# Optimization experiments

Measured on AMD Instinct MI355X. Metric: run time of the kernel, lower is better.

Reference implementation:

```python
import jax, jax.numpy as jnp
import numpy as np
from jax import lax


def quick_gelu(x):
    return x * jax.nn.sigmoid(1.702 * x)


def setup_inputs() -> dict:
    key = jax.random.key(0)
    ks = jax.random.split(key, 12)
    B, H, W, C, D, M = 32, 56, 56, 192, 64, 8
    g = lambda k, shape, s: (jax.random.normal(k, shape, jnp.float32) * s)
    return {
        "x": jax.random.normal(ks[0], (B, H, W, C), jnp.float32),
        "W1": g(ks[1], (64, C), 0.05),
        "b1": jnp.zeros((64,), jnp.float32),
        "W2": g(ks[2], (64, 64), 0.05),
        "b2": jnp.zeros((64,), jnp.float32),
        "mask_token": g(ks[3], (M, 64), 0.05),
        "Wh": g(ks[4], (D * D * 9, 64), 0.02),
        "bh": g(ks[5], (D * D * 9,), 0.02),
        "Wd": g(ks[6], (D, C), 0.05),
        "bd": jnp.zeros((D,), jnp.float32),
        "Wu": g(ks[7], (C, D), 0.02),
        "bu": jnp.zeros((C,), jnp.float32),
    }


def reference(x, W1, b1, W2, b2, mask_token, Wh, bh, Wd, bd, Wu, bu):
    B, H, W_, C = x.shape
    D = Wd.shape[0]
    M = mask_token.shape[0]
    # meta_net: Linear -> ReLU -> Linear, [B,H,W,64]
    pf = jax.nn.relu(jnp.einsum("bhwc,kc->bhwk", x, W1) + b1)
    pf = jnp.einsum("bhwk,jk->bhwj", pf, W2) + b2
    # mask routing: [M,B,H,W], softmax over spatial positions
    mask = jnp.einsum("bhwk,mk->mbhw", pf, mask_token)
    mask = jax.nn.softmax(mask.reshape(M, B, -1), axis=-1).reshape(M, B, H, W_)
    # sum_m mask[m][...,None]*pf, then sum over H,W -> [B,64]
    mwf = (mask.sum(0)[..., None] * pf).sum(axis=(1, 2))
    # hypernet: per-sample conv weights [B,D,D,3,3]
    conv_w = (jnp.einsum("bk,ok->bo", mwf, Wh) + bh).reshape(B, D, D, 3, 3)
    # adapter_down + QuickGELU, [B,D,H,W]
    xd = jnp.einsum("bhwc,dc->bhwd", x, Wd) + bd
    xp = quick_gelu(xd.transpose(0, 3, 1, 2))

    def conv1(xi, wi):  # xi [D,H,W], wi [D,D,3,3]
        return lax.conv_general_dilated(xi[None], wi, (1, 1), [(1, 1), (1, 1)])[0]

    xc = jax.vmap(conv1)(xp, conv_w)  # [B,D,H,W]
    xd2 = quick_gelu(xc.transpose(0, 2, 3, 1))  # [B,H,W,D]
    # dropout(p=0.1) is identity in eval mode
    xu = jnp.einsum("bhwd,cd->bhwc", xd2, Wu) + bu
    return xu + x
```

## Files before the change

kernel.cpp:

```cpp
#include <hip/hip_runtime.h>

typedef unsigned short ushort_t;
typedef short bf16x8 __attribute__((ext_vector_type(8)));
typedef float f32x4 __attribute__((ext_vector_type(4)));

#define MFMA(a, b, c) __builtin_amdgcn_mfma_f32_16x16x32_bf16(a, b, c, 0, 0, 0)

#define B_    32
#define HW_   3136
#define NPOS  100352

__device__ __forceinline__ float bf2f(unsigned short h) {
    return __uint_as_float(((unsigned int)h) << 16);
}
__device__ __forceinline__ unsigned short f2bf(float f) {
    unsigned int u = __float_as_uint(f);
    u += 0x7FFFu + ((u >> 16) & 1u);
    return (unsigned short)(u >> 16);
}
__device__ __forceinline__ float qgelu(float v) {
    return v / (1.0f + __expf(-1.702f * v));
}
__device__ __forceinline__ void unpack8(uint4 v, float* f) {
    f[0] = bf2f((unsigned short)(v.x & 0xffff)); f[1] = bf2f((unsigned short)(v.x >> 16));
    f[2] = bf2f((unsigned short)(v.y & 0xffff)); f[3] = bf2f((unsigned short)(v.y >> 16));
    f[4] = bf2f((unsigned short)(v.z & 0xffff)); f[5] = bf2f((unsigned short)(v.z >> 16));
    f[6] = bf2f((unsigned short)(v.w & 0xffff)); f[7] = bf2f((unsigned short)(v.w >> 16));
}

__global__ __launch_bounds__(256) void k0_prep(
    const float* __restrict__ W1, const float* __restrict__ W2,
    const float* __restrict__ mtok, const float* __restrict__ Wd,
    const float* __restrict__ Wu,
    ushort_t* __restrict__ w1f, ushort_t* __restrict__ wdf,
    ushort_t* __restrict__ w2f, ushort_t* __restrict__ mtf,
    ushort_t* __restrict__ wuf)
{
    const int gid = blockIdx.x * 256 + threadIdx.x;
    const int stride = gridDim.x * 256;
    for (int i = gid; i < 12288; i += stride) {
        int j = i & 7, lane = (i >> 3) & 63, nt = (i >> 9) & 3, kc = i >> 11;
        int n = nt * 16 + (lane & 15), k = kc * 32 + (lane >> 4) * 8 + j;
        w1f[i] = f2bf(W1[n * 192 + k]);
        wdf[i] = f2bf(Wd[n * 192 + k]);
    }
    for (int i = gid; i < 4096; i += stride) {
        int j = i & 7, lane = (i >> 3) & 63, nt = (i >> 9) & 3, kc = i >> 11;
        int n = nt * 16 + (lane & 15), k = kc * 32 + (lane >> 4) * 8 + j;
        w2f[i] = f2bf(W2[n * 64 + k]);
    }
    for (int i = gid; i < 1024; i += stride) {
        int j = i & 7, lane = (i >> 3) & 63, kc = i >> 9;
        int n = lane & 15, k = kc * 32 + (lane >> 4) * 8 + j;
        mtf[i] = (n < 8) ? f2bf(mtok[n * 64 + k]) : (ushort_t)0;
    }
    for (int i = gid; i < 12288; i += stride) {
        int j = i & 7, lane = (i >> 3) & 63, g = i >> 9;
        int nt = g % 12, kc = g / 12;
        int n = nt * 16 + (lane & 15), k = kc * 32 + (lane >> 4) * 8 + j;
        wuf[i] = f2bf(Wu[n * 64 + k]);
    }
}

__global__ __launch_bounds__(64, 2) void k1_meta_adapter(
    const float* __restrict__ x, const float* __restrict__ b1,
    const float* __restrict__ b2, const float* __restrict__ bd,
    const ushort_t* __restrict__ w1f, const ushort_t* __restrict__ wdf,
    const ushort_t* __restrict__ w2f, const ushort_t* __restrict__ mtf,
    ushort_t* __restrict__ pf2g, ushort_t* __restrict__ xpg,
    float* __restrict__ Lg)
{
    __shared__ ushort_t buf[16 * 72];

    const int lane = threadIdx.x;
    const int col = lane & 15, q = lane >> 4;
    const int posBase = blockIdx.x * 64;

    float bias1[4], biasd[4], bias2[4];
    #pragma unroll
    for (int nt = 0; nt < 4; nt++) {
        bias1[nt] = b1[nt * 16 + col];
        biasd[nt] = bd[nt * 16 + col];
        bias2[nt] = b2[nt * 16 + col];
    }

    f32x4 acc1[4][4], acc3[4][4];
    #pragma unroll
    for (int m = 0; m < 4; m++)
        #pragma unroll
        for (int nt = 0; nt < 4; nt++) { acc1[m][nt] = (f32x4)0.0f; acc3[m][nt] = (f32x4)0.0f; }

    #pragma unroll
    for (int kc = 0; kc < 6; kc++) {
        bf16x8 A[4];
        #pragma unroll
        for (int m = 0; m < 4; m++) {
            const float4* gp = (const float4*)(x +
                (size_t)(posBase + m * 16 + col) * 192 + kc * 32 + q * 8);
            float4 v0 = gp[0], v1 = gp[1];
            A[m][0] = (short)f2bf(v0.x); A[m][1] = (short)f2bf(v0.y);
            A[m][2] = (short)f2bf(v0.z); A[m][3] = (short)f2bf(v0.w);
            A[m][4] = (short)f2bf(v1.x); A[m][5] = (short)f2bf(v1.y);
            A[m][6] = (short)f2bf(v1.z); A[m][7] = (short)f2bf(v1.w);
        }
        #pragma unroll
        for (int nt = 0; nt < 4; nt++) {
            bf16x8 B1 = *(const bf16x8*)(w1f + ((kc * 4 + nt) * 64 + lane) * 8);
            #pragma unroll
            for (int m = 0; m < 4; m++) acc1[m][nt] = MFMA(A[m], B1, acc1[m][nt]);
            bf16x8 Bd = *(const bf16x8*)(wdf + ((kc * 4 + nt) * 64 + lane) * 8);
            #pragma unroll
            for (int m = 0; m < 4; m++) acc3[m][nt] = MFMA(A[m], Bd, acc3[m][nt]);
        }
    }

    #pragma unroll
    for (int m = 0; m < 4; m++) {
        const int rowBase = posBase + m * 16;

        #pragma unroll
        for (int nt = 0; nt < 4; nt++)
            #pragma unroll
            for (int r = 0; r < 4; r++) {
                float v = acc1[m][nt][r] + bias1[nt];
                v = v > 0.0f ? v : 0.0f;
                buf[(q * 4 + r) * 72 + nt * 16 + col] = f2bf(v);
            }

        f32x4 acc2[4];
        #pragma unroll
        for (int nt = 0; nt < 4; nt++) acc2[nt] = (f32x4)0.0f;
        #pragma unroll
        for (int kc = 0; kc < 2; kc++) {
            bf16x8 A2 = *(const bf16x8*)&buf[col * 72 + kc * 32 + q * 8];
            #pragma unroll
            for (int nt = 0; nt < 4; nt++) {
                bf16x8 B2 = *(const bf16x8*)(w2f + ((kc * 4 + nt) * 64 + lane) * 8);
                acc2[nt] = MFMA(A2, B2, acc2[nt]);
            }
        }

        #pragma unroll
        for (int nt = 0; nt < 4; nt++)
            #pragma unroll
            for (int r = 0; r < 4; r++) {
                float v = qgelu(acc3[m][nt][r] + biasd[nt]);
                buf[(q * 4 + r) * 72 + nt * 16 + col] = f2bf(v);
            }

        #pragma unroll
        for (int t = 0; t < 2; t++) {
            int idx = lane + t * 64;
            int pos = idx >> 3, c8 = idx & 7;
            uint4 vx = *(const uint4*)&buf[pos * 72 + c8 * 8];
            *(uint4*)(xpg + ((size_t)(rowBase + pos)) * 64 + c8 * 8) = vx;
        }

        #pragma unroll
        for (int nt = 0; nt < 4; nt++)
            #pragma unroll
            for (int r = 0; r < 4; r++)
                buf[(q * 4 + r) * 72 + nt * 16 + col] = f2bf(acc2[nt][r] + bias2[nt]);

        f32x4 Lacc = (f32x4)0.0f;
        #pragma unroll
        for (int kc = 0; kc < 2; kc++) {
            bf16x8 A3 = *(const bf16x8*)&buf[col * 72 + kc * 32 + q * 8];
            bf16x8 Bm = *(const bf16x8*)(mtf + (kc * 64 + lane) * 8);
            Lacc = MFMA(A3, Bm, Lacc);
        }
        if (col < 8) {
            #pragma unroll
            for (int r = 0; r < 4; r++)
                Lg[((size_t)(rowBase + q * 4 + r)) * 8 + col] = Lacc[r];
        }

        #pragma unroll
        for (int t = 0; t < 2; t++) {
            int idx = lane + t * 64;
            int pos = idx >> 3, c8 = idx & 7;
            uint4 vp = *(const uint4*)&buf[pos * 72 + c8 * 8];
            *(uint4*)(pf2g + ((size_t)(rowBase + pos)) * 64 + c8 * 8) = vp;
        }
    }
}

__global__ __launch_bounds__(256) void k2a_partial(
    const float* __restrict__ Lg, float* __restrict__ Pmax, float* __restrict__ Psum)
{
    __shared__ float wred[4][8];
    __shared__ float Msh[8];

    const int tid = threadIdx.x;
    const int b = blockIdx.x >> 3, sl = blockIdx.x & 7;
    const int lane = tid & 63, wv = tid >> 6;
    const float* Lb = Lg + ((size_t)b * HW_ + (size_t)sl * 392) * 8;

    float l0[8], l1[8];
    {
        const float4* p = (const float4*)(Lb + (size_t)tid * 8);
        float4 a = p[0], c = p[1];
        l0[0] = a.x; l0[1] = a.y; l0[2] = a.z; l0[3] = a.w;
        l0[4] = c.x; l0[5] = c.y; l0[6] = c.z; l0[7] = c.w;
    }
    if (tid < 136) {
        const float4* p = (const float4*)(Lb + (size_t)(tid + 256) * 8);
        float4 a = p[0], c = p[1];
        l1[0] = a.x; l1[1] = a.y; l1[2] = a.z; l1[3] = a.w;
        l1[4] = c.x; l1[5] = c.y; l1[6] = c.z; l1[7] = c.w;
    } else {
        #pragma unroll
        for (int m = 0; m < 8; m++) l1[m] = -1e30f;
    }

    float lm[8];
    #pragma unroll
    for (int m = 0; m < 8; m++) {
        float v = fmaxf(l0[m], l1[m]);
        for (int off = 32; off > 0; off >>= 1) v = fmaxf(v, __shfl_down(v, off));
        lm[m] = v;
    }
    if (lane == 0) {
        #pragma unroll
        for (int m = 0; m < 8; m++) wred[wv][m] = lm[m];
    }
    __syncthreads();
    if (tid < 8)
        Msh[tid] = fmaxf(fmaxf(wred[0][tid], wred[1][tid]), fmaxf(wred[2][tid], wred[3][tid]));
    __syncthreads();

    float s[8];
    #pragma unroll
    for (int m = 0; m < 8; m++)
        s[m] = __expf(l0[m] - Msh[m]) + __expf(l1[m] - Msh[m]);
    #pragma unroll
    for (int m = 0; m < 8; m++) {
        float v = s[m];
        for (int off = 32; off > 0; off >>= 1) v += __shfl_down(v, off);
        s[m] = v;
    }
    __syncthreads();
    if (lane == 0) {
        #pragma unroll
        for (int m = 0; m < 8; m++) wred[wv][m] = s[m];
    }
    __syncthreads();
    if (tid < 8) {
        Psum[((size_t)b * 8 + sl) * 8 + tid] =
            wred[0][tid] + wred[1][tid] + wred[2][tid] + wred[3][tid];
        Pmax[((size_t)b * 8 + sl) * 8 + tid] = Msh[tid];
    }
}

__global__ __launch_bounds__(256) void k2b_combine(
    const float* __restrict__ Pmax, const float* __restrict__ Psum,
    float* __restrict__ smxg, float* __restrict__ sinvg, float* __restrict__ mwfg)
{
    const int tid = threadIdx.x;
    const int b = tid >> 3, m = tid & 7;
    float M = -1e30f;
    #pragma unroll
    for (int sl = 0; sl < 8; sl++)
        M = fmaxf(M, Pmax[((size_t)b * 8 + sl) * 8 + m]);
    float S = 0.0f;
    #pragma unroll
    for (int sl = 0; sl < 8; sl++)
        S += Psum[((size_t)b * 8 + sl) * 8 + m] * __expf(Pmax[((size_t)b * 8 + sl) * 8 + m] - M);
    smxg[tid] = M;
    sinvg[tid] = 1.0f / S;
    for (int i = tid; i < 2048; i += 256) mwfg[i] = 0.0f;
}

__global__ __launch_bounds__(256) void k2c_mwf(
    const float* __restrict__ Lg, const ushort_t* __restrict__ pf2g,
    const float* __restrict__ smxg, const float* __restrict__ sinvg,
    float* __restrict__ mwfg)
{
    __shared__ float ms[392];
    __shared__ float sred[32 * 64];

    const int tid = threadIdx.x;
    const int b = blockIdx.x >> 3, sl = blockIdx.x & 7;
    const size_t base = (size_t)b * HW_ + (size_t)sl * 392;

    float smx[8], sinv[8];
    #pragma unroll
    for (int m = 0; m < 8; m++) {
        smx[m] = smxg[b * 8 + m];
        sinv[m] = sinvg[b * 8 + m];
    }

    for (int lp = tid; lp < 392; lp += 256) {
        const float4* p = (const float4*)(Lg + (base + lp) * 8);
        float4 a = p[0], c = p[1];
        ms[lp] = __expf(a.x - smx[0]) * sinv[0] + __expf(a.y - smx[1]) * sinv[1]
               + __expf(a.z - smx[2]) * sinv[2] + __expf(a.w - smx[3]) * sinv[3]
               + __expf(c.x - smx[4]) * sinv[4] + __expf(c.y - smx[5]) * sinv[5]
               + __expf(c.z - smx[6]) * sinv[6] + __expf(c.w - smx[7]) * sinv[7];
    }
    __syncthreads();

    const int part = tid >> 3, kg = tid & 7;
    float a8[8];
    #pragma unroll
    for (int j = 0; j < 8; j++) a8[j] = 0.0f;
    for (int lp = part; lp < 392; lp += 32) {
        float w = ms[lp];
        uint4 v = *(const uint4*)(pf2g + (base + lp) * 64 + kg * 8);
        float f[8]; unpack8(v, f);
        #pragma unroll
        for (int j = 0; j < 8; j++) a8[j] += w * f[j];
    }
    #pragma unroll
    for (int j = 0; j < 8; j++) sred[part * 64 + kg * 8 + j] = a8[j];
    __syncthreads();
    if (tid < 64) {
        float s = 0.0f;
        #pragma unroll
        for (int pt = 0; pt < 32; pt++) s += sred[pt * 64 + tid];
        atomicAdd(&mwfg[b * 64 + tid], s);
    }
}

__global__ __launch_bounds__(256) void k3_hypernet(
    const float* __restrict__ mwfg, const float* __restrict__ Whg,
    const float* __restrict__ bhg, ushort_t* __restrict__ cwb)
{
    __shared__ float mwfs[32 * 64];
    const int tid = threadIdx.x;
    for (int i = tid; i < 2048; i += 256) mwfs[i] = mwfg[i];
    __syncthreads();

    const int op = blockIdx.x * 64 + (tid >> 2);
    const int bq = tid & 3;
    const int j = op & 7, lane = (op >> 3) & 63, nt = (op >> 9) & 3;
    const int kc = (op >> 11) & 1, tap = op >> 12;
    const int oc = nt * 16 + (lane & 15);
    const int ic = kc * 32 + (lane >> 4) * 8 + j;
    const int o = oc * 576 + ic * 9 + tap;

    float wreg[64];
    const float4* src = (const float4*)(Whg + (size_t)o * 64);
    #pragma unroll
    for (int t = 0; t < 16; t++) {
        float4 v = src[t];
        wreg[t * 4 + 0] = v.x; wreg[t * 4 + 1] = v.y;
        wreg[t * 4 + 2] = v.z; wreg[t * 4 + 3] = v.w;
    }
    const float bias = bhg[o];
    #pragma unroll
    for (int i = 0; i < 8; i += 2) {
        int b0 = bq * 8 + i, b1 = b0 + 1;
        float a0 = bias, a1 = bias;
        #pragma unroll
        for (int k = 0; k < 64; k++) {
            a0 += mwfs[b0 * 64 + k] * wreg[k];
            a1 += mwfs[b1 * 64 + k] * wreg[k];
        }
        cwb[(size_t)b0 * 36864 + op] = f2bf(a0);
        cwb[(size_t)b1 * 36864 + op] = f2bf(a1);
    }
}

__global__ __launch_bounds__(256, 4) void k4_conv(
    const ushort_t* __restrict__ xpg, const ushort_t* __restrict__ cwb,
    ushort_t* __restrict__ xd2g)
{
    __shared__ ushort_t xs[2 * 232 * 40];

    const int tid = threadIdx.x;
    const int bid = blockIdx.x;
    const int swz = (bid & 7) * 112 + (bid >> 3);
    const int b = swz / 28, yt = swz % 28, y0 = yt * 2;

    for (int u = tid; u < 1856; u += 256) {
        int r = u / 464, rem = u % 464, c = rem >> 3, c8 = rem & 7;
        int gy = y0 - 1 + r, gx = c - 1;
        uint4 v = make_uint4(0, 0, 0, 0);
        if (gy >= 0 && gy < 56 && gx >= 0 && gx < 56)
            v = *(const uint4*)(xpg + ((size_t)b * HW_ + gy * 56 + gx) * 64 + c8 * 8);
        int kc = c8 >> 2, q = c8 & 3;
        *(uint4*)&xs[kc * 9280 + (r * 58 + c) * 40 + q * 8] = v;
    }
    __syncthreads();

    const int lane = tid & 63, wv = tid >> 6;
    const int col = lane & 15, q = lane >> 4;

    int abase[7];
    #pragma unroll
    for (int t = 0; t < 7; t++) {
        int p = t * 16 + col;
        int row = p / 56, cc = p - row * 56;
        abase[t] = ((row * 58 + cc) * 40 + q * 8) * 2;
    }

    f32x4 acc[7];
    #pragma unroll
    for (int t = 0; t < 7; t++) acc[t] = (f32x4)0.0f;

    const ushort_t* wbase = cwb + (size_t)b * 36864;
    #pragma unroll
    for (int tap = 0; tap < 9; tap++) {
        const int dy = tap / 3, dx = tap % 3;
        const int toff = (dy * 58 + dx) * 80;
        bf16x8 Bf0 = *(const bf16x8*)(wbase + tap * 4096 + ((0 * 4 + wv) * 64 + lane) * 8);
        bf16x8 Bf1 = *(const bf16x8*)(wbase + tap * 4096 + ((1 * 4 + wv) * 64 + lane) * 8);
        #pragma unroll
        for (int t = 0; t < 7; t++) {
            bf16x8 A0 = *(const bf16x8*)((const char*)xs + abase[t] + toff);
            bf16x8 A1 = *(const bf16x8*)((const char*)xs + 18560 + abase[t] + toff);
            acc[t] = MFMA(A0, Bf0, acc[t]);
            acc[t] = MFMA(A1, Bf1, acc[t]);
        }
    }
    __syncthreads();

    #pragma unroll
    for (int t = 0; t < 7; t++)
        #pragma unroll
        for (int r = 0; r < 4; r++)
            xs[(t * 16 + q * 4 + r) * 72 + wv * 16 + col] = f2bf(qgelu(acc[t][r]));
    __syncthreads();

    for (int u = tid; u < 896; u += 256) {
        int pos = u >> 3, c8 = u & 7;
        uint4 v = *(const uint4*)&xs[pos * 72 + c8 * 8];
        size_t gpos = (size_t)b * HW_ + (size_t)y0 * 56 + pos;
        *(uint4*)(xd2g + gpos * 64 + c8 * 8) = v;
    }
}

__global__ __launch_bounds__(256, 4) void k5_up_res(
    const ushort_t* __restrict__ xd2g, const ushort_t* __restrict__ wuf,
    const float* __restrict__ bu, const float* __restrict__ xg,
    float* __restrict__ outg)
{
    __shared__ ushort_t xds[64 * 72];
    __shared__ ushort_t wsh[12288];

    const int tid = threadIdx.x;
    const size_t posBase = (size_t)blockIdx.x * 64;

    {
        uint4* d = (uint4*)wsh;
        const uint4* s = (const uint4*)wuf;
        for (int u = tid; u < 1536; u += 256) d[u] = s[u];
    }
    #pragma unroll
    for (int t = 0; t < 2; t++) {
        int u = tid + t * 256;
        int pos = u >> 3, c8 = u & 7;
        uint4 v = *(const uint4*)(xd2g + (posBase + pos) * 64 + c8 * 8);
        *(uint4*)&xds[pos * 72 + c8 * 8] = v;
    }
    __syncthreads();

    const int lane = tid & 63, wv = tid >> 6;
    const int col = lane & 15, q = lane >> 4;

    bf16x8 A[2];
    #pragma unroll
    for (int kc = 0; kc < 2; kc++)
        A[kc] = *(const bf16x8*)&xds[(wv * 16 + col) * 72 + kc * 32 + q * 8];

    f32x4 acc[12];
    #pragma unroll
    for (int nt = 0; nt < 12; nt++) acc[nt] = (f32x4)0.0f;
    #pragma unroll
    for (int kc = 0; kc < 2; kc++)
        #pragma unroll
        for (int nt = 0; nt < 12; nt++) {
            bf16x8 B = *(const bf16x8*)&wsh[((kc * 12 + nt) * 64 + lane) * 8];
            acc[nt] = MFMA(A[kc], B, acc[nt]);
        }

    #pragma unroll
    for (int nt = 0; nt < 12; nt++) {
        float bias = bu[nt * 16 + col];
        #pragma unroll
        for (int r = 0; r < 4; r++) {
            size_t off = (posBase + wv * 16 + q * 4 + r) * 192 + nt * 16 + col;
            outg[off] = acc[nt][r] + bias + xg[off];
        }
    }
}

extern "C" void kernel_launch(void* const* d_in, const int* in_sizes, int n_in,
                              void* d_out, int out_size, void* d_ws, size_t ws_size,
                              hipStream_t stream) {
    const float* x    = (const float*)d_in[0];
    const float* W1   = (const float*)d_in[1];
    const float* b1   = (const float*)d_in[2];
    const float* W2   = (const float*)d_in[3];
    const float* b2   = (const float*)d_in[4];
    const float* mtok = (const float*)d_in[5];
    const float* Wh   = (const float*)d_in[6];
    const float* bh   = (const float*)d_in[7];
    const float* Wd   = (const float*)d_in[8];
    const float* bd   = (const float*)d_in[9];
    const float* Wu   = (const float*)d_in[10];
    const float* bu   = (const float*)d_in[11];
    float* out = (float*)d_out;

    char* ws = (char*)d_ws;
    ushort_t* pf2 = (ushort_t*)ws;
    ushort_t* xp  = (ushort_t*)(ws + 12845056);
    ushort_t* xd2 = pf2;
    ushort_t* cwb = (ushort_t*)(ws + 25690112);
    float*    mwf = (float*)(ws + 28049408);
    float*    Lg  = (float*)(ws + 28057600);
    ushort_t* w1f = (ushort_t*)(ws + 31268864);
    ushort_t* wdf = (ushort_t*)(ws + 31293440);
    ushort_t* w2f = (ushort_t*)(ws + 31318016);
    ushort_t* mtf = (ushort_t*)(ws + 31326208);
    ushort_t* wuf = (ushort_t*)(ws + 31328256);
    float*    Pmax= (float*)(ws + 31352832);
    float*    Psum= (float*)(ws + 31361024);
    float*    smxg= (float*)(ws + 31369216);
    float*    sinvg=(float*)(ws + 31370240);

    k0_prep<<<48, 256, 0, stream>>>(W1, W2, mtok, Wd, Wu, w1f, wdf, w2f, mtf, wuf);
    k1_meta_adapter<<<1568, 64, 0, stream>>>(x, b1, b2, bd, w1f, wdf, w2f, mtf,
                                             pf2, xp, Lg);
    k2a_partial<<<256, 256, 0, stream>>>(Lg, Pmax, Psum);
    k2b_combine<<<1, 256, 0, stream>>>(Pmax, Psum, smxg, sinvg, mwf);
    k2c_mwf<<<256, 256, 0, stream>>>(Lg, pf2, smxg, sinvg, mwf);
    k3_hypernet<<<576, 256, 0, stream>>>(mwf, Wh, bh, cwb);
    k4_conv<<<896, 256, 0, stream>>>(xp, cwb, xd2);
    k5_up_res<<<1568, 256, 0, stream>>>(xd2, wuf, bu, x, out);
}
```

Baseline: 241.3 us.

## Split meta/adapter and up-projection across four waves; fold softmax combine kernel

k1 moves from one 64-thread wave per 64 positions to four waves, each owning a 16-column output slice, with weights held in registers and intermediates passed through shared memory. The tiny k2b combine kernel is removed: k2c now recomputes the per-batch max and sum from the partials, and the mwf zeroing moves into k2a. k5 drops its shared-memory staging and has each wave load weights and activations straight from global memory, with the register tile reshaped to 4 row blocks by 3 column blocks. In exchange, every wave in k1 re-reads the same x rows (four times the L2 traffic for x, with repeated bf16 conversion), and k5 loses its shared weight staging.

```diff
diff --git a/kernel.cpp b/kernel.cpp
--- a/kernel.cpp
+++ b/kernel.cpp
@@ -62,7 +62,7 @@
     }
 }
 
-__global__ __launch_bounds__(64, 2) void k1_meta_adapter(
+__global__ __launch_bounds__(256, 2) void k1_meta_adapter(
     const float* __restrict__ x, const float* __restrict__ b1,
     const float* __restrict__ b2, const float* __restrict__ bd,
     const ushort_t* __restrict__ w1f, const ushort_t* __restrict__ wdf,
@@ -70,25 +70,34 @@
     ushort_t* __restrict__ pf2g, ushort_t* __restrict__ xpg,
     float* __restrict__ Lg)
 {
-    __shared__ ushort_t buf[16 * 72];
-
-    const int lane = threadIdx.x;
+    __shared__ ushort_t pf1s[64 * 72];
+    __shared__ ushort_t pf2s[64 * 72];
+    __shared__ ushort_t xps[64 * 72];
+
+    const int tid = threadIdx.x;
+    const int lane = tid & 63, wv = tid >> 6;
     const int col = lane & 15, q = lane >> 4;
     const int posBase = blockIdx.x * 64;
 
-    float bias1[4], biasd[4], bias2[4];
-    #pragma unroll
-    for (int nt = 0; nt < 4; nt++) {
-        bias1[nt] = b1[nt * 16 + col];
-        biasd[nt] = bd[nt * 16 + col];
-        bias2[nt] = b2[nt * 16 + col];
-    }
-
-    f32x4 acc1[4][4], acc3[4][4];
-    #pragma unroll
-    for (int m = 0; m < 4; m++)
-        #pragma unroll
-        for (int nt = 0; nt < 4; nt++) { acc1[m][nt] = (f32x4)0.0f; acc3[m][nt] = (f32x4)0.0f; }
+    bf16x8 B1r[6], Bdr[6], B2r[2], Bmr[2];
+    #pragma unroll
+    for (int kc = 0; kc < 6; kc++) {
+        B1r[kc] = *(const bf16x8*)(w1f + ((kc * 4 + wv) * 64 + lane) * 8);
+        Bdr[kc] = *(const bf16x8*)(wdf + ((kc * 4 + wv) * 64 + lane) * 8);
+    }
+    #pragma unroll
+    for (int kc = 0; kc < 2; kc++) {
+        B2r[kc] = *(const bf16x8*)(w2f + ((kc * 4 + wv) * 64 + lane) * 8);
+        Bmr[kc] = *(const bf16x8*)(mtf + (kc * 64 + lane) * 8);
+    }
+
+    const float bias1 = b1[wv * 16 + col];
+    const float biasd = bd[wv * 16 + col];
+    const float bias2 = b2[wv * 16 + col];
+
+    f32x4 acc1[4], acc3[4];
+    #pragma unroll
+    for (int m = 0; m < 4; m++) { acc1[m] = (f32x4)0.0f; acc3[m] = (f32x4)0.0f; }
 
     #pragma unroll
     for (int kc = 0; kc < 6; kc++) {
@@ -104,89 +113,69 @@
             A[m][6] = (short)f2bf(v1.z); A[m][7] = (short)f2bf(v1.w);
         }
         #pragma unroll
-        for (int nt = 0; nt < 4; nt++) {
-            bf16x8 B1 = *(const bf16x8*)(w1f + ((kc * 4 + nt) * 64 + lane) * 8);
-            #pragma unroll
-            for (int m = 0; m < 4; m++) acc1[m][nt] = MFMA(A[m], B1, acc1[m][nt]);
-            bf16x8 Bd = *(const bf16x8*)(wdf + ((kc * 4 + nt) * 64 + lane) * 8);
-            #pragma unroll
-            for (int m = 0; m < 4; m++) acc3[m][nt] = MFMA(A[m], Bd, acc3[m][nt]);
+        for (int m = 0; m < 4; m++) {
+            acc1[m] = MFMA(A[m], B1r[kc], acc1[m]);
+            acc3[m] = MFMA(A[m], Bdr[kc], acc3[m]);
         }
     }
 
     #pragma unroll
-    for (int m = 0; m < 4; m++) {
-        const int rowBase = posBase + m * 16;
-
-        #pragma unroll
-        for (int nt = 0; nt < 4; nt++)
-            #pragma unroll
-            for (int r = 0; r < 4; r++) {
-                float v = acc1[m][nt][r] + bias1[nt];
-                v = v > 0.0f ? v : 0.0f;
-                buf[(q * 4 + r) * 72 + nt * 16 + col] = f2bf(v);
-            }
-
-        f32x4 acc2[4];
-        #pragma unroll
-        for (int nt = 0; nt < 4; nt++) acc2[nt] = (f32x4)0.0f;
-        #pragma unroll
-        for (int kc = 0; kc < 2; kc++) {
-            bf16x8 A2 = *(const bf16x8*)&buf[col * 72 + kc * 32 + q * 8];
-            #pragma unroll
-            for (int nt = 0; nt < 4; nt++) {
-                bf16x8 B2 = *(const bf16x8*)(w2f + ((kc * 4 + nt) * 64 + lane) * 8);
-                acc2[nt] = MFMA(A2, B2, acc2[nt]);
-            }
+    for (int m = 0; m < 4; m++)
+        #pragma unroll
+        for (int r = 0; r < 4; r++)
+            pf1s[(m * 16 + q * 4 + r) * 72 + wv * 16 + col] =
+                f2bf(fmaxf(acc1[m][r] + bias1, 0.0f));
+    __syncthreads();
+
+    f32x4 acc2[4];
+    #pragma unroll
+    for (int m = 0; m < 4; m++) acc2[m] = (f32x4)0.0f;
+    #pragma unroll
+    for (int kc = 0; kc < 2; kc++) {
+        #pragma unroll
+        for (int m = 0; m < 4; m++) {
+            bf16x8 A2 = *(const bf16x8*)&pf1s[(m * 16 + col) * 72 + kc * 32 + q * 8];
+            acc2[m] = MFMA(A2, B2r[kc], acc2[m]);
         }
-
-        #pragma unroll
-        for (int nt = 0; nt < 4; nt++)
-            #pragma unroll
-            for (int r = 0; r < 4; r++) {
-                float v = qgelu(acc3[m][nt][r] + biasd[nt]);
-                buf[(q * 4 + r) * 72 + nt * 16 + col] = f2bf(v);
-            }
-
-        #pragma unroll
-        for (int t = 0; t < 2; t++) {
-            int idx = lane + t * 64;
-            int pos = idx >> 3, c8 = idx & 7;
-            uint4 vx = *(const uint4*)&buf[pos * 72 + c8 * 8];
-            *(uint4*)(xpg + ((size_t)(rowBase + pos)) * 64 + c8 * 8) = vx;
+    }
+
+    #pragma unroll
+    for (int m = 0; m < 4; m++)
+        #pragma unroll
+        for (int r = 0; r < 4; r++) {
+            xps[(m * 16 + q * 4 + r) * 72 + wv * 16 + col] =
+                f2bf(qgelu(acc3[m][r] + biasd));
+            pf2s[(m * 16 + q * 4 + r) * 72 + wv * 16 + col] =
+                f2bf(acc2[m][r] + bias2);
         }
-
-        #pragma unroll
-        for (int nt = 0; nt < 4; nt++)
-            #pragma unroll
-            for (int r = 0; r < 4; r++)
-                buf[(q * 4 + r) * 72 + nt * 16 + col] = f2bf(acc2[nt][r] + bias2[nt]);
-
-        f32x4 Lacc = (f32x4)0.0f;
-        #pragma unroll
-        for (int kc = 0; kc < 2; kc++) {
-            bf16x8 A3 = *(const bf16x8*)&buf[col * 72 + kc * 32 + q * 8];
-            bf16x8 Bm = *(const bf16x8*)(mtf + (kc * 64 + lane) * 8);
-            Lacc = MFMA(A3, Bm, Lacc);
-        }
-        if (col < 8) {
-            #pragma unroll
-            for (int r = 0; r < 4; r++)
-                Lg[((size_t)(rowBase + q * 4 + r)) * 8 + col] = Lacc[r];
-        }
-
-        #pragma unroll
-        for (int t = 0; t < 2; t++) {
-            int idx = lane + t * 64;
-            int pos = idx >> 3, c8 = idx & 7;
-            uint4 vp = *(const uint4*)&buf[pos * 72 + c8 * 8];
-            *(uint4*)(pf2g + ((size_t)(rowBase + pos)) * 64 + c8 * 8) = vp;
-        }
+    __syncthreads();
+
+    f32x4 Lacc = (f32x4)0.0f;
+    #pragma unroll
+    for (int kc = 0; kc < 2; kc++) {
+        bf16x8 A3 = *(const bf16x8*)&pf2s[(wv * 16 + col) * 72 + kc * 32 + q * 8];
+        Lacc = MFMA(A3, Bmr[kc], Lacc);
+    }
+    if (col < 8) {
+        #pragma unroll
+        for (int r = 0; r < 4; r++)
+            Lg[((size_t)(posBase + wv * 16 + q * 4 + r)) * 8 + col] = Lacc[r];
+    }
+
+    #pragma unroll
+    for (int t = 0; t < 2; t++) {
+        int u = tid + t * 256;
+        int pos = u >> 3, c8 = u & 7;
+        uint4 vx = *(const uint4*)&xps[pos * 72 + c8 * 8];
+        *(uint4*)(xpg + ((size_t)(posBase + pos)) * 64 + c8 * 8) = vx;
+        uint4 vp = *(const uint4*)&pf2s[pos * 72 + c8 * 8];
+        *(uint4*)(pf2g + ((size_t)(posBase + pos)) * 64 + c8 * 8) = vp;
     }
 }
 
 __global__ __launch_bounds__(256) void k2a_partial(
-    const float* __restrict__ Lg, float* __restrict__ Pmax, float* __restrict__ Psum)
+    const float* __restrict__ Lg, float* __restrict__ Pmax, float* __restrict__ Psum,
+    float* __restrict__ mwfg)
 {
     __shared__ float wred[4][8];
     __shared__ float Msh[8];
@@ -195,6 +184,9 @@
     const int b = blockIdx.x >> 3, sl = blockIdx.x & 7;
     const int lane = tid & 63, wv = tid >> 6;
     const float* Lb = Lg + ((size_t)b * HW_ + (size_t)sl * 392) * 8;
+
+    if (blockIdx.x == 0)
+        for (int i = tid; i < 2048; i += 256) mwfg[i] = 0.0f;
 
     float l0[8], l1[8];
     {
@@ -252,28 +244,9 @@
     }
 }
 
-__global__ __launch_bounds__(256) void k2b_combine(
-    const float* __restrict__ Pmax, const float* __restrict__ Psum,
-    float* __restrict__ smxg, float* __restrict__ sinvg, float* __restrict__ mwfg)
-{
-    const int tid = threadIdx.x;
-    const int b = tid >> 3, m = tid & 7;
-    float M = -1e30f;
-    #pragma unroll
-    for (int sl = 0; sl < 8; sl++)
-        M = fmaxf(M, Pmax[((size_t)b * 8 + sl) * 8 + m]);
-    float S = 0.0f;
-    #pragma unroll
-    for (int sl = 0; sl < 8; sl++)
-        S += Psum[((size_t)b * 8 + sl) * 8 + m] * __expf(Pmax[((size_t)b * 8 + sl) * 8 + m] - M);
-    smxg[tid] = M;
-    sinvg[tid] = 1.0f / S;
-    for (int i = tid; i < 2048; i += 256) mwfg[i] = 0.0f;
-}
-
 __global__ __launch_bounds__(256) void k2c_mwf(
     const float* __restrict__ Lg, const ushort_t* __restrict__ pf2g,
-    const float* __restrict__ smxg, const float* __restrict__ sinvg,
+    const float* __restrict__ Pmax, const float* __restrict__ Psum,
     float* __restrict__ mwfg)
 {
     __shared__ float ms[392];
@@ -286,8 +259,16 @@
     float smx[8], sinv[8];
     #pragma unroll
     for (int m = 0; m < 8; m++) {
-        smx[m] = smxg[b * 8 + m];
-        sinv[m] = sinvg[b * 8 + m];
+        float M = -1e30f;
+        #pragma unroll
+        for (int s2 = 0; s2 < 8; s2++)
+            M = fmaxf(M, Pmax[((size_t)b * 8 + s2) * 8 + m]);
+        float S = 0.0f;
+        #pragma unroll
+        for (int s2 = 0; s2 < 8; s2++)
+            S += Psum[((size_t)b * 8 + s2) * 8 + m] *
+                 __expf(Pmax[((size_t)b * 8 + s2) * 8 + m] - M);
+        smx[m] = M; sinv[m] = 1.0f / S;
     }
 
     for (int lp = tid; lp < 392; lp += 256) {
@@ -431,59 +412,58 @@
     }
 }
 
-__global__ __launch_bounds__(256, 4) void k5_up_res(
+__global__ __launch_bounds__(256, 2) void k5_up_res(
     const ushort_t* __restrict__ xd2g, const ushort_t* __restrict__ wuf,
     const float* __restrict__ bu, const float* __restrict__ xg,
     float* __restrict__ outg)
 {
-    __shared__ ushort_t xds[64 * 72];
-    __shared__ ushort_t wsh[12288];
-
     const int tid = threadIdx.x;
-    const size_t posBase = (size_t)blockIdx.x * 64;
-
-    {
-        uint4* d = (uint4*)wsh;
-        const uint4* s = (const uint4*)wuf;
-        for (int u = tid; u < 1536; u += 256) d[u] = s[u];
-    }
-    #pragma unroll
-    for (int t = 0; t < 2; t++) {
-        int u = tid + t * 256;
-        int pos = u >> 3, c8 = u & 7;
-        uint4 v = *(const uint4*)(xd2g + (posBase + pos) * 64 + c8 * 8);
-        *(uint4*)&xds[pos * 72 + c8 * 8] = v;
-    }
-    __syncthreads();
-
     const int lane = tid & 63, wv = tid >> 6;
     const int col = lane & 15, q = lane >> 4;
-
-    bf16x8 A[2];
+    const size_t posBase = (size_t)blockIdx.x * 64;
+
+    bf16x8 Bw[2][3];
     #pragma unroll
     for (int kc = 0; kc < 2; kc++)
-        A[kc] = *(const bf16x8*)&xds[(wv * 16 + col) * 72 + kc * 32 + q * 8];
-
-    f32x4 acc[12];
-    #pragma unroll
-    for (int nt = 0; nt < 12; nt++) acc[nt] = (f32x4)0.0f;
+        #pragma unroll
+        for (int nt = 0; nt < 3; nt++)
+            Bw[kc][nt] = *(const bf16x8*)(wuf + ((kc * 12 + wv * 3 + nt) * 64 + lane) * 8);
+
+    bf16x8 A[4][2];
+    #pragma unroll
+    for (int m = 0; m < 4; m++)
+        #pragma unroll
+        for (int kc = 0; kc < 2; kc++)
+            A[m][kc] = *(const bf16x8*)(xd2g +
+                (posBase + m * 16 + col) * 64 + kc * 32 + q * 8);
+
+    float biasu[3];
+    #pragma unroll
+    for (int nt = 0; nt < 3; nt++) biasu[nt] = bu[(wv * 3 + nt) * 16 + col];
+
+    f32x4 acc[4][3];
+    #pragma unroll
+    for (int m = 0; m < 4; m++)
+        #pragma unroll
+        for (int nt = 0; nt < 3; nt++) acc[m][nt] = (f32x4)0.0f;
+
     #pragma unroll
     for (int kc = 0; kc < 2; kc++)
         #pragma unroll
-        for (int nt = 0; nt < 12; nt++) {
-            bf16x8 B = *(const bf16x8*)&wsh[((kc * 12 + nt) * 64 + lane) * 8];
-            acc[nt] = MFMA(A[kc], B, acc[nt]);
-        }
-
-    #pragma unroll
-    for (int nt = 0; nt < 12; nt++) {
-        float bias = bu[nt * 16 + col];
-        #pragma unroll
-        for (int r = 0; r < 4; r++) {
-            size_t off = (posBase + wv * 16 + q * 4 + r) * 192 + nt * 16 + col;
-            outg[off] = acc[nt][r] + bias + xg[off];
-        }
-    }
+        for (int m = 0; m < 4; m++)
+            #pragma unroll
+            for (int nt = 0; nt < 3; nt++)
+                acc[m][nt] = MFMA(A[m][kc], Bw[kc][nt], acc[m][nt]);
+
+    #pragma unroll
+    for (int m = 0; m < 4; m++)
+        #pragma unroll
+        for (int nt = 0; nt < 3; nt++)
+            #pragma unroll
+            for (int r = 0; r < 4; r++) {
+                size_t off = (posBase + m * 16 + q * 4 + r) * 192 + (wv * 3 + nt) * 16 + col;
+                outg[off] = acc[m][nt][r] + biasu[nt] + xg[off];
+            }
 }
 
 extern "C" void kernel_launch(void* const* d_in, const int* in_sizes, int n_in,
@@ -517,15 +497,12 @@
     ushort_t* wuf = (ushort_t*)(ws + 31328256);
     float*    Pmax= (float*)(ws + 31352832);
     float*    Psum= (float*)(ws + 31361024);
-    float*    smxg= (float*)(ws + 31369216);
-    float*    sinvg=(float*)(ws + 31370240);
 
     k0_prep<<<48, 256, 0, stream>>>(W1, W2, mtok, Wd, Wu, w1f, wdf, w2f, mtf, wuf);
-    k1_meta_adapter<<<1568, 64, 0, stream>>>(x, b1, b2, bd, w1f, wdf, w2f, mtf,
-                                             pf2, xp, Lg);
-    k2a_partial<<<256, 256, 0, stream>>>(Lg, Pmax, Psum);
-    k2b_combine<<<1, 256, 0, stream>>>(Pmax, Psum, smxg, sinvg, mwf);
-    k2c_mwf<<<256, 256, 0, stream>>>(Lg, pf2, smxg, sinvg, mwf);
+    k1_meta_adapter<<<1568, 256, 0, stream>>>(x, b1, b2, bd, w1f, wdf, w2f, mtf,
+                                              pf2, xp, Lg);
+    k2a_partial<<<256, 256, 0, stream>>>(Lg, Pmax, Psum, mwf);
+    k2c_mwf<<<256, 256, 0, stream>>>(Lg, pf2, Pmax, Psum, mwf);
     k3_hypernet<<<576, 256, 0, stream>>>(mwf, Wh, bh, cwb);
     k4_conv<<<896, 256, 0, stream>>>(xp, cwb, xd2);
     k5_up_res<<<1568, 256, 0, stream>>>(xd2, wuf, bu, x, out);
```

New measurement: 256.4 us. 1.06x slower.

## Fuse block-local softmax and weighted pf reduction into meta kernel

Applied to the files above, without the earlier changes.

The meta/adapter kernel now keeps its 64 positions' pf2 tile and routing logits in shared memory. It computes a block-local online-softmax max and sum, plus a per-mask weighted pf sum via MFMA, and writes only small per-block partials. A single combine kernel rescales those partials into mwf. This drops the global pf2 and logit round trips and replaces three launches with one. The cost is more LDS per block and the removal of the occupancy hint, and the exp weights are rounded to bf16 before the MFMA.

```diff
diff --git a/kernel.cpp b/kernel.cpp
--- a/kernel.cpp
+++ b/kernel.cpp
@@ -20,12 +20,6 @@
 }
 __device__ __forceinline__ float qgelu(float v) {
     return v / (1.0f + __expf(-1.702f * v));
-}
-__device__ __forceinline__ void unpack8(uint4 v, float* f) {
-    f[0] = bf2f((unsigned short)(v.x & 0xffff)); f[1] = bf2f((unsigned short)(v.x >> 16));
-    f[2] = bf2f((unsigned short)(v.y & 0xffff)); f[3] = bf2f((unsigned short)(v.y >> 16));
-    f[4] = bf2f((unsigned short)(v.z & 0xffff)); f[5] = bf2f((unsigned short)(v.z >> 16));
-    f[6] = bf2f((unsigned short)(v.w & 0xffff)); f[7] = bf2f((unsigned short)(v.w >> 16));
 }
 
 __global__ __launch_bounds__(256) void k0_prep(
@@ -62,19 +56,23 @@
     }
 }
 
-__global__ __launch_bounds__(64, 2) void k1_meta_adapter(
+__global__ __launch_bounds__(64) void k1_meta_adapter(
     const float* __restrict__ x, const float* __restrict__ b1,
     const float* __restrict__ b2, const float* __restrict__ bd,
     const ushort_t* __restrict__ w1f, const ushort_t* __restrict__ wdf,
     const ushort_t* __restrict__ w2f, const ushort_t* __restrict__ mtf,
-    ushort_t* __restrict__ pf2g, ushort_t* __restrict__ xpg,
-    float* __restrict__ Lg)
+    ushort_t* __restrict__ xpg, float* __restrict__ Tg, float* __restrict__ MSg)
 {
     __shared__ ushort_t buf[16 * 72];
+    __shared__ ushort_t pf2t[64 * 72];
+    __shared__ ushort_t wsh[16 * 72];
+    __shared__ float    Lsh[64 * 8];
 
     const int lane = threadIdx.x;
     const int col = lane & 15, q = lane >> 4;
     const int posBase = blockIdx.x * 64;
+
+    for (int i = lane; i < 576; i += 64) wsh[8 * 72 + i] = 0;
 
     float bias1[4], biasd[4], bias2[4];
     #pragma unroll
@@ -147,7 +145,6 @@
                 float v = qgelu(acc3[m][nt][r] + biasd[nt]);
                 buf[(q * 4 + r) * 72 + nt * 16 + col] = f2bf(v);
             }
-
         #pragma unroll
         for (int t = 0; t < 2; t++) {
             int idx = lane + t * 64;
@@ -157,10 +154,19 @@
         }
 
         #pragma unroll
-        for (int nt = 0; nt < 4; nt++)
-            #pragma unroll
-            for (int r = 0; r < 4; r++)
-                buf[(q * 4 + r) * 72 + nt * 16 + col] = f2bf(acc2[nt][r] + bias2[nt]);
+        for (int nt = 0; nt < 4; nt++) {
+            ushort_t h[4];
+            #pragma unroll
+            for (int r = 0; r < 4; r++) {
+                float v = acc2[nt][r] + bias2[nt];
+                h[r] = f2bf(v);
+                buf[(q * 4 + r) * 72 + nt * 16 + col] = h[r];
+            }
+            unsigned int p01 = (unsigned int)h[0] | ((unsigned int)h[1] << 16);
+            unsigned int p23 = (unsigned int)h[2] | ((unsigned int)h[3] << 16);
+            unsigned int* dst = (unsigned int*)&pf2t[(nt * 16 + col) * 72 + m * 16 + q * 4];
+            dst[0] = p01; dst[1] = p23;
+        }
 
         f32x4 Lacc = (f32x4)0.0f;
         #pragma unroll
@@ -172,154 +178,91 @@
         if (col < 8) {
             #pragma unroll
             for (int r = 0; r < 4; r++)
-                Lg[((size_t)(rowBase + q * 4 + r)) * 8 + col] = Lacc[r];
-        }
-
-        #pragma unroll
-        for (int t = 0; t < 2; t++) {
-            int idx = lane + t * 64;
-            int pos = idx >> 3, c8 = idx & 7;
-            uint4 vp = *(const uint4*)&buf[pos * 72 + c8 * 8];
-            *(uint4*)(pf2g + ((size_t)(rowBase + pos)) * 64 + c8 * 8) = vp;
-        }
-    }
-}
-
-__global__ __launch_bounds__(256) void k2a_partial(
-    const float* __restrict__ Lg, float* __restrict__ Pmax, float* __restrict__ Psum)
-{
-    __shared__ float wred[4][8];
-    __shared__ float Msh[8];
+                Lsh[(m * 16 + q * 4 + r) * 8 + col] = Lacc[r];
+        }
+    }
+
+    float4 La = *(const float4*)&Lsh[lane * 8];
+    float4 Lb = *(const float4*)&Lsh[lane * 8 + 4];
+    float l[8] = {La.x, La.y, La.z, La.w, Lb.x, Lb.y, Lb.z, Lb.w};
+    float Mb[8], Sb[8];
+    #pragma unroll
+    for (int m = 0; m < 8; m++) {
+        float v = l[m];
+        #pragma unroll
+        for (int off = 32; off > 0; off >>= 1) v = fmaxf(v, __shfl_xor(v, off));
+        Mb[m] = v;
+        float e = __expf(l[m] - v);
+        wsh[m * 72 + lane] = f2bf(e);
+        float s = e;
+        #pragma unroll
+        for (int off = 32; off > 0; off >>= 1) s += __shfl_xor(s, off);
+        Sb[m] = s;
+    }
+
+    f32x4 tac[4];
+    #pragma unroll
+    for (int mt = 0; mt < 4; mt++) tac[mt] = (f32x4)0.0f;
+    #pragma unroll
+    for (int kc = 0; kc < 2; kc++) {
+        bf16x8 Bw = *(const bf16x8*)&wsh[col * 72 + kc * 32 + q * 8];
+        #pragma unroll
+        for (int mt = 0; mt < 4; mt++) {
+            bf16x8 Ap = *(const bf16x8*)&pf2t[(mt * 16 + col) * 72 + kc * 32 + q * 8];
+            tac[mt] = MFMA(Ap, Bw, tac[mt]);
+        }
+    }
+    if (col < 8) {
+        #pragma unroll
+        for (int mt = 0; mt < 4; mt++)
+            *(f32x4*)(Tg + (size_t)blockIdx.x * 512 + col * 64 + mt * 16 + q * 4) = tac[mt];
+    }
+    if (lane < 8) {
+        MSg[blockIdx.x * 16 + lane] = Mb[lane];
+        MSg[blockIdx.x * 16 + 8 + lane] = Sb[lane];
+    }
+}
+
+__global__ __launch_bounds__(256) void k2_combine(
+    const float* __restrict__ Tg, const float* __restrict__ MSg,
+    float* __restrict__ mwfg)
+{
+    __shared__ float smx[8], sinv[8];
+    __shared__ float fac[49][8];
+    __shared__ float sred[4][64];
 
     const int tid = threadIdx.x;
-    const int b = blockIdx.x >> 3, sl = blockIdx.x & 7;
-    const int lane = tid & 63, wv = tid >> 6;
-    const float* Lb = Lg + ((size_t)b * HW_ + (size_t)sl * 392) * 8;
-
-    float l0[8], l1[8];
-    {
-        const float4* p = (const float4*)(Lb + (size_t)tid * 8);
-        float4 a = p[0], c = p[1];
-        l0[0] = a.x; l0[1] = a.y; l0[2] = a.z; l0[3] = a.w;
-        l0[4] = c.x; l0[5] = c.y; l0[6] = c.z; l0[7] = c.w;
-    }
-    if (tid < 136) {
-        const float4* p = (const float4*)(Lb + (size_t)(tid + 256) * 8);
-        float4 a = p[0], c = p[1];
-        l1[0] = a.x; l1[1] = a.y; l1[2] = a.z; l1[3] = a.w;
-        l1[4] = c.x; l1[5] = c.y; l1[6] = c.z; l1[7] = c.w;
-    } else {
-        #pragma unroll
-        for (int m = 0; m < 8; m++) l1[m] = -1e30f;
-    }
-
-    float lm[8];
-    #pragma unroll
-    for (int m = 0; m < 8; m++) {
-        float v = fmaxf(l0[m], l1[m]);
-        for (int off = 32; off > 0; off >>= 1) v = fmaxf(v, __shfl_down(v, off));
-        lm[m] = v;
-    }
-    if (lane == 0) {
-        #pragma unroll
-        for (int m = 0; m < 8; m++) wred[wv][m] = lm[m];
-    }
-    __syncthreads();
-    if (tid < 8)
-        Msh[tid] = fmaxf(fmaxf(wred[0][tid], wred[1][tid]), fmaxf(wred[2][tid], wred[3][tid]));
-    __syncthreads();
-
-    float s[8];
-    #pragma unroll
-    for (int m = 0; m < 8; m++)
-        s[m] = __expf(l0[m] - Msh[m]) + __expf(l1[m] - Msh[m]);
-    #pragma unroll
-    for (int m = 0; m < 8; m++) {
-        float v = s[m];
-        for (int off = 32; off > 0; off >>= 1) v += __shfl_down(v, off);
-        s[m] = v;
-    }
-    __syncthreads();
-    if (lane == 0) {
-        #pragma unroll
-        for (int m = 0; m < 8; m++) wred[wv][m] = s[m];
-    }
-    __syncthreads();
+    const int b = blockIdx.x;
+    const int base = b * 49;
+
     if (tid < 8) {
-        Psum[((size_t)b * 8 + sl) * 8 + tid] =
-            wred[0][tid] + wred[1][tid] + wred[2][tid] + wred[3][tid];
-        Pmax[((size_t)b * 8 + sl) * 8 + tid] = Msh[tid];
-    }
-}
-
-__global__ __launch_bounds__(256) void k2b_combine(
-    const float* __restrict__ Pmax, const float* __restrict__ Psum,
-    float* __restrict__ smxg, float* __restrict__ sinvg, float* __restrict__ mwfg)
-{
-    const int tid = threadIdx.x;
-    const int b = tid >> 3, m = tid & 7;
-    float M = -1e30f;
-    #pragma unroll
-    for (int sl = 0; sl < 8; sl++)
-        M = fmaxf(M, Pmax[((size_t)b * 8 + sl) * 8 + m]);
-    float S = 0.0f;
-    #pragma unroll
-    for (int sl = 0; sl < 8; sl++)
-        S += Psum[((size_t)b * 8 + sl) * 8 + m] * __expf(Pmax[((size_t)b * 8 + sl) * 8 + m] - M);
-    smxg[tid] = M;
-    sinvg[tid] = 1.0f / S;
-    for (int i = tid; i < 2048; i += 256) mwfg[i] = 0.0f;
-}
-
-__global__ __launch_bounds__(256) void k2c_mwf(
-    const float* __restrict__ Lg, const ushort_t* __restrict__ pf2g,
-    const float* __restrict__ smxg, const float* __restrict__ sinvg,
-    float* __restrict__ mwfg)
-{
-    __shared__ float ms[392];
-    __shared__ float sred[32 * 64];
-
-    const int tid = threadIdx.x;
-    const int b = blockIdx.x >> 3, sl = blockIdx.x & 7;
-    const size_t base = (size_t)b * HW_ + (size_t)sl * 392;
-
-    float smx[8], sinv[8];
-    #pragma unroll
-    for (int m = 0; m < 8; m++) {
-        smx[m] = smxg[b * 8 + m];
-        sinv[m] = sinvg[b * 8 + m];
-    }
-
-    for (int lp = tid; lp < 392; lp += 256) {
-        const float4* p = (const float4*)(Lg + (base + lp) * 8);
-        float4 a = p[0], c = p[1];
-        ms[lp] = __expf(a.x - smx[0]) * sinv[0] + __expf(a.y - smx[1]) * sinv[1]
-               + __expf(a.z - smx[2]) * sinv[2] + __expf(a.w - smx[3]) * sinv[3]
-               + __expf(c.x - smx[4]) * sinv[4] + __expf(c.y - smx[5]) * sinv[5]
-               + __expf(c.z - smx[6]) * sinv[6] + __expf(c.w - smx[7]) * sinv[7];
-    }
-    __syncthreads();
-
-    const int part = tid >> 3, kg = tid & 7;
-    float a8[8];
-    #pragma unroll
-    for (int j = 0; j < 8; j++) a8[j] = 0.0f;
-    for (int lp = part; lp < 392; lp += 32) {
-        float w = ms[lp];
-        uint4 v = *(const uint4*)(pf2g + (base + lp) * 64 + kg * 8);
-        float f[8]; unpack8(v, f);
-        #pragma unroll
-        for (int j = 0; j < 8; j++) a8[j] += w * f[j];
-    }
-    #pragma unroll
-    for (int j = 0; j < 8; j++) sred[part * 64 + kg * 8 + j] = a8[j];
-    __syncthreads();
-    if (tid < 64) {
-        float s = 0.0f;
-        #pragma unroll
-        for (int pt = 0; pt < 32; pt++) s += sred[pt * 64 + tid];
-        atomicAdd(&mwfg[b * 64 + tid], s);
-    }
+        float M = -1e30f;
+        for (int blk = 0; blk < 49; blk++)
+            M = fmaxf(M, MSg[(base + blk) * 16 + tid]);
+        float S = 0.0f;
+        for (int blk = 0; blk < 49; blk++)
+            S += MSg[(base + blk) * 16 + 8 + tid] *
+                 __expf(MSg[(base + blk) * 16 + tid] - M);
+        smx[tid] = M;
+        sinv[tid] = 1.0f / S;
+    }
+    __syncthreads();
+    for (int i = tid; i < 392; i += 256) {
+        int blk = i >> 3, m = i & 7;
+        fac[blk][m] = __expf(MSg[(base + blk) * 16 + m] - smx[m]) * sinv[m];
+    }
+    __syncthreads();
+
+    const int k = tid & 63, mg = tid >> 6;
+    float t = 0.0f;
+    for (int blk = 0; blk < 49; blk++) {
+        const float* Tb = Tg + (size_t)(base + blk) * 512;
+        t += fac[blk][mg] * Tb[mg * 64 + k] + fac[blk][mg + 4] * Tb[(mg + 4) * 64 + k];
+    }
+    sred[mg][k] = t;
+    __syncthreads();
+    if (tid < 64)
+        mwfg[b * 64 + tid] = sred[0][tid] + sred[1][tid] + sred[2][tid] + sred[3][tid];
 }
 
 __global__ __launch_bounds__(256) void k3_hypernet(
@@ -504,28 +447,22 @@
     float* out = (float*)d_out;
 
     char* ws = (char*)d_ws;
-    ushort_t* pf2 = (ushort_t*)ws;
+    float*    MSg = (float*)ws;
+    ushort_t* xd2 = (ushort_t*)ws;
     ushort_t* xp  = (ushort_t*)(ws + 12845056);
-    ushort_t* xd2 = pf2;
     ushort_t* cwb = (ushort_t*)(ws + 25690112);
     float*    mwf = (float*)(ws + 28049408);
-    float*    Lg  = (float*)(ws + 28057600);
+    float*    Tg  = (float*)(ws + 28057600);
     ushort_t* w1f = (ushort_t*)(ws + 31268864);
     ushort_t* wdf = (ushort_t*)(ws + 31293440);
     ushort_t* w2f = (ushort_t*)(ws + 31318016);
     ushort_t* mtf = (ushort_t*)(ws + 31326208);
     ushort_t* wuf = (ushort_t*)(ws + 31328256);
-    float*    Pmax= (float*)(ws + 31352832);
-    float*    Psum= (float*)(ws + 31361024);
-    float*    smxg= (float*)(ws + 31369216);
-    float*    sinvg=(float*)(ws + 31370240);
 
     k0_prep<<<48, 256, 0, stream>>>(W1, W2, mtok, Wd, Wu, w1f, wdf, w2f, mtf, wuf);
     k1_meta_adapter<<<1568, 64, 0, stream>>>(x, b1, b2, bd, w1f, wdf, w2f, mtf,
-                                             pf2, xp, Lg);
-    k2a_partial<<<256, 256, 0, stream>>>(Lg, Pmax, Psum);
-    k2b_combine<<<1, 256, 0, stream>>>(Pmax, Psum, smxg, sinvg, mwf);
-    k2c_mwf<<<256, 256, 0, stream>>>(Lg, pf2, smxg, sinvg, mwf);
+                                             xp, Tg, MSg);
+    k2_combine<<<32, 256, 0, stream>>>(Tg, MSg, mwf);
     k3_hypernet<<<576, 256, 0, stream>>>(mwf, Wh, bh, cwb);
     k4_conv<<<896, 256, 0, stream>>>(xp, cwb, xd2);
     k5_up_res<<<1568, 256, 0, stream>>>(xd2, wuf, bu, x, out);
```

Result: slower. 261.9 us (+8.6%).

## Fuse up-projection and residual into conv kernel; stage hypernet weights in LDS

Applied to the files above, without the earlier changes.

The 3x3 conv kernel now computes the Wu up-projection, bias and residual add directly from its LDS tile of QuickGELU outputs. This removes the xd2 intermediate round trip through global memory and one kernel launch. The hypernet kernel loads each Wh row cooperatively into padded shared memory instead of into 64 registers per thread, which lowers register pressure at the cost of extra LDS traffic. The fused conv kernel reads Wu fragments straight from global or L2 without an LDS copy, and each block now writes 112 positions of 192 fp32 channels.

```diff
diff --git a/kernel.cpp b/kernel.cpp
--- a/kernel.cpp
+++ b/kernel.cpp
@@ -147,7 +147,6 @@
                 float v = qgelu(acc3[m][nt][r] + biasd[nt]);
                 buf[(q * 4 + r) * 72 + nt * 16 + col] = f2bf(v);
             }
-
         #pragma unroll
         for (int t = 0; t < 2; t++) {
             int idx = lane + t * 64;
@@ -326,27 +325,36 @@
     const float* __restrict__ mwfg, const float* __restrict__ Whg,
     const float* __restrict__ bhg, ushort_t* __restrict__ cwb)
 {
-    __shared__ float mwfs[32 * 64];
+    __shared__ float mwfs[32 * 66];
+    __shared__ float wrow[64][65];
+
     const int tid = threadIdx.x;
-    for (int i = tid; i < 2048; i += 256) mwfs[i] = mwfg[i];
-    __syncthreads();
-
-    const int op = blockIdx.x * 64 + (tid >> 2);
-    const int bq = tid & 3;
+    for (int i = tid; i < 2048; i += 256) {
+        int b = i >> 6, k = i & 63;
+        mwfs[b * 66 + k] = mwfg[i];
+    }
+
+    const int ol = tid >> 2, bq = tid & 3;
+    const int op = blockIdx.x * 64 + ol;
     const int j = op & 7, lane = (op >> 3) & 63, nt = (op >> 9) & 3;
     const int kc = (op >> 11) & 1, tap = op >> 12;
     const int oc = nt * 16 + (lane & 15);
     const int ic = kc * 32 + (lane >> 4) * 8 + j;
     const int o = oc * 576 + ic * 9 + tap;
 
-    float wreg[64];
-    const float4* src = (const float4*)(Whg + (size_t)o * 64);
-    #pragma unroll
-    for (int t = 0; t < 16; t++) {
-        float4 v = src[t];
-        wreg[t * 4 + 0] = v.x; wreg[t * 4 + 1] = v.y;
-        wreg[t * 4 + 2] = v.z; wreg[t * 4 + 3] = v.w;
-    }
+    {
+        const float4* src = (const float4*)(Whg + (size_t)o * 64 + bq * 16);
+        #pragma unroll
+        for (int t = 0; t < 4; t++) {
+            float4 v = src[t];
+            wrow[ol][bq * 16 + t * 4 + 0] = v.x;
+            wrow[ol][bq * 16 + t * 4 + 1] = v.y;
+            wrow[ol][bq * 16 + t * 4 + 2] = v.z;
+            wrow[ol][bq * 16 + t * 4 + 3] = v.w;
+        }
+    }
+    __syncthreads();
+
     const float bias = bhg[o];
     #pragma unroll
     for (int i = 0; i < 8; i += 2) {
@@ -354,17 +362,19 @@
         float a0 = bias, a1 = bias;
         #pragma unroll
         for (int k = 0; k < 64; k++) {
-            a0 += mwfs[b0 * 64 + k] * wreg[k];
-            a1 += mwfs[b1 * 64 + k] * wreg[k];
+            float w = wrow[ol][k];
+            a0 += mwfs[b0 * 66 + k] * w;
+            a1 += mwfs[b1 * 66 + k] * w;
         }
         cwb[(size_t)b0 * 36864 + op] = f2bf(a0);
         cwb[(size_t)b1 * 36864 + op] = f2bf(a1);
     }
 }
 
-__global__ __launch_bounds__(256, 4) void k4_conv(
+__global__ __launch_bounds__(256, 4) void k4_conv_up(
     const ushort_t* __restrict__ xpg, const ushort_t* __restrict__ cwb,
-    ushort_t* __restrict__ xd2g)
+    const ushort_t* __restrict__ wuf, const float* __restrict__ bu,
+    const float* __restrict__ xg, float* __restrict__ outg)
 {
     __shared__ ushort_t xs[2 * 232 * 40];
 
@@ -423,66 +433,30 @@
             xs[(t * 16 + q * 4 + r) * 72 + wv * 16 + col] = f2bf(qgelu(acc[t][r]));
     __syncthreads();
 
-    for (int u = tid; u < 896; u += 256) {
-        int pos = u >> 3, c8 = u & 7;
-        uint4 v = *(const uint4*)&xs[pos * 72 + c8 * 8];
-        size_t gpos = (size_t)b * HW_ + (size_t)y0 * 56 + pos;
-        *(uint4*)(xd2g + gpos * 64 + c8 * 8) = v;
-    }
-}
-
-__global__ __launch_bounds__(256, 4) void k5_up_res(
-    const ushort_t* __restrict__ xd2g, const ushort_t* __restrict__ wuf,
-    const float* __restrict__ bu, const float* __restrict__ xg,
-    float* __restrict__ outg)
-{
-    __shared__ ushort_t xds[64 * 72];
-    __shared__ ushort_t wsh[12288];
-
-    const int tid = threadIdx.x;
-    const size_t posBase = (size_t)blockIdx.x * 64;
-
-    {
-        uint4* d = (uint4*)wsh;
-        const uint4* s = (const uint4*)wuf;
-        for (int u = tid; u < 1536; u += 256) d[u] = s[u];
-    }
-    #pragma unroll
-    for (int t = 0; t < 2; t++) {
-        int u = tid + t * 256;
-        int pos = u >> 3, c8 = u & 7;
-        uint4 v = *(const uint4*)(xd2g + (posBase + pos) * 64 + c8 * 8);
-        *(uint4*)&xds[pos * 72 + c8 * 8] = v;
-    }
-    __syncthreads();
-
-    const int lane = tid & 63, wv = tid >> 6;
-    const int col = lane & 15, q = lane >> 4;
-
-    bf16x8 A[2];
-    #pragma unroll
-    for (int kc = 0; kc < 2; kc++)
-        A[kc] = *(const bf16x8*)&xds[(wv * 16 + col) * 72 + kc * 32 + q * 8];
-
-    f32x4 acc[12];
-    #pragma unroll
-    for (int nt = 0; nt < 12; nt++) acc[nt] = (f32x4)0.0f;
-    #pragma unroll
-    for (int kc = 0; kc < 2; kc++)
-        #pragma unroll
-        for (int nt = 0; nt < 12; nt++) {
-            bf16x8 B = *(const bf16x8*)&wsh[((kc * 12 + nt) * 64 + lane) * 8];
-            acc[nt] = MFMA(A[kc], B, acc[nt]);
-        }
-
-    #pragma unroll
-    for (int nt = 0; nt < 12; nt++) {
-        float bias = bu[nt * 16 + col];
-        #pragma unroll
-        for (int r = 0; r < 4; r++) {
-            size_t off = (posBase + wv * 16 + q * 4 + r) * 192 + nt * 16 + col;
-            outg[off] = acc[nt][r] + bias + xg[off];
-        }
+    const size_t rowG = (size_t)b * HW_ + (size_t)y0 * 56;
+    #pragma unroll
+    for (int nt = 0; nt < 3; nt++) {
+        const int ncol = (wv * 3 + nt) * 16 + col;
+        const float bias = bu[ncol];
+        f32x4 accu[7];
+        #pragma unroll
+        for (int mt = 0; mt < 7; mt++) accu[mt] = (f32x4)0.0f;
+        #pragma unroll
+        for (int kc = 0; kc < 2; kc++) {
+            bf16x8 Bw = *(const bf16x8*)(wuf + ((kc * 12 + wv * 3 + nt) * 64 + lane) * 8);
+            #pragma unroll
+            for (int mt = 0; mt < 7; mt++) {
+                bf16x8 A = *(const bf16x8*)&xs[(mt * 16 + col) * 72 + kc * 32 + q * 8];
+                accu[mt] = MFMA(A, Bw, accu[mt]);
+            }
+        }
+        #pragma unroll
+        for (int mt = 0; mt < 7; mt++)
+            #pragma unroll
+            for (int r = 0; r < 4; r++) {
+                size_t off = (rowG + mt * 16 + q * 4 + r) * 192 + ncol;
+                outg[off] = accu[mt][r] + bias + xg[off];
+            }
     }
 }
 
@@ -506,7 +480,6 @@
     char* ws = (char*)d_ws;
     ushort_t* pf2 = (ushort_t*)ws;
     ushort_t* xp  = (ushort_t*)(ws + 12845056);
-    ushort_t* xd2 = pf2;
     ushort_t* cwb = (ushort_t*)(ws + 25690112);
     float*    mwf = (float*)(ws + 28049408);
     float*    Lg  = (float*)(ws + 28057600);
@@ -527,6 +500,5 @@
     k2b_combine<<<1, 256, 0, stream>>>(Pmax, Psum, smxg, sinvg, mwf);
     k2c_mwf<<<256, 256, 0, stream>>>(Lg, pf2, smxg, sinvg, mwf);
     k3_hypernet<<<576, 256, 0, stream>>>(mwf, Wh, bh, cwb);
-    k4_conv<<<896, 256, 0, stream>>>(xp, cwb, xd2);
-    k5_up_res<<<1568, 256, 0, stream>>>(xd2, wuf, bu, x, out);
-}
+    k4_conv_up<<<896, 256, 0, stream>>>(xp, cwb, wuf, bu, x, out);
+}
```

After: 251.9 us. 4.4% more time.
